# Optimization experiments

Hardware: AMD Instinct MI355X
Metric: run time of the kernel (lower is better)

The kernel has to match this reference:

```python
import math
import jax, jax.numpy as jnp
import numpy as np

N_HEADS = 16
CHUNK = 64  # sqrt(S) block size for the Cron-Root (sqrt-decomposition) branch


def _chunked_causal_attention(q, k, v, chunk=CHUNK):
    """Exact causal softmax attention computed in sqrt-size query blocks.

    Math-equivalent to F.scaled_dot_product_attention(q,k,v,is_causal=True),
    but never materializes the full [B,H,S,S] score matrix (honors the
    sqrt-decomposition structure of cron_root_attention_v14).
    q,k,v: [B,H,S,D] -> out [B,H,S,D]
    """
    B, H, S, D = q.shape
    scale = 1.0 / math.sqrt(D)
    nc = S // chunk
    qc = jnp.moveaxis(q.reshape(B, H, nc, chunk, D), 2, 0)  # [nc,B,H,C,D]
    kpos = jnp.arange(S)

    def body(_, inp):
        qi, ci = inp  # qi: [B,H,C,D], ci: scalar chunk index
        scores = jnp.einsum('bhcd,bhsd->bhcs', qi, k) * scale  # [B,H,C,S]
        qpos = ci * chunk + jnp.arange(chunk)
        mask = kpos[None, :] <= qpos[:, None]  # [C,S] causal
        scores = jnp.where(mask, scores, jnp.finfo(scores.dtype).min)
        p = jax.nn.softmax(scores, axis=-1)
        return None, jnp.einsum('bhcs,bhsd->bhcd', p, v)

    _, outs = jax.lax.scan(body, None, (qc, jnp.arange(nc)))  # [nc,B,H,C,D]
    return jnp.moveaxis(outs, 0, 2).reshape(B, H, S, D)


def setup_inputs() -> dict:
    key = jax.random.key(0)
    kx, kq, kk, kv, ko = jax.random.split(key, 5)
    d = 1024
    x = jax.random.normal(kx, (1, 4096, d), dtype=jnp.float32)
    # nn.Linear weights are [out_features, in_features]; no bias (bias=False)
    Wq = jax.random.normal(kq, (d, d), dtype=jnp.float32) * 0.02
    Wk = jax.random.normal(kk, (d, d), dtype=jnp.float32) * 0.02
    Wv = jax.random.normal(kv, (d, d), dtype=jnp.float32) * 0.02
    Wo = jax.random.normal(ko, (d, d), dtype=jnp.float32) * 0.02
    return {"x": x, "Wq": Wq, "Wk": Wk, "Wv": Wv, "Wo": Wo}


def reference(x, Wq, Wk, Wv, Wo):
    B, S, D = x.shape
    H = N_HEADS
    hd = D // H
    # projections (torch Linear: y = x @ W.T)
    q = (x @ Wq.T).reshape(B, S, H, hd).transpose(0, 2, 1, 3)
    k = (x @ Wk.T).reshape(B, S, H, hd).transpose(0, 2, 1, 3)
    v = (x @ Wv.T).reshape(B, S, H, hd).transpose(0, 2, 1, 3)
    # S=4096 >= threshold=1536 -> cron_root branch (exact causal attention)
    out = _chunked_causal_attention(q, k, v)
    out = out.transpose(0, 2, 1, 3).reshape(B, S, D)
    return out @ Wo.T
```

## Files before the change

### kernel.cpp

```cpp
#include <hip/hip_runtime.h>
#include <math.h>

#define S_LEN  4096
#define DMODEL 1024
#define NH     16
#define HD     64

typedef __bf16 bf16;
typedef __attribute__((ext_vector_type(8))) __bf16 bf16x8;
typedef __attribute__((ext_vector_type(4))) float  f32x4;

__device__ inline void gl_lds16(const void* g, void* l) {
    __builtin_amdgcn_global_load_lds(
        (const __attribute__((address_space(1))) void*)g,
        (__attribute__((address_space(3))) void*)l, 16, 0, 0);
}

__global__ __launch_bounds__(256)
void f32_to_bf16_all(const float* __restrict__ x,  const float* __restrict__ wq,
                     const float* __restrict__ wk, const float* __restrict__ wv,
                     const float* __restrict__ wo,
                     bf16* __restrict__ xb,  bf16* __restrict__ wqb,
                     bf16* __restrict__ wkb, bf16* __restrict__ wvb,
                     bf16* __restrict__ wob)
{
    int b = blockIdx.x;
    const float* s; bf16* d; int idx;
    if      (b < 2048) { s = x;  d = xb;  idx = b; }
    else if (b < 2560) { s = wq; d = wqb; idx = b - 2048; }
    else if (b < 3072) { s = wk; d = wkb; idx = b - 2560; }
    else if (b < 3584) { s = wv; d = wvb; idx = b - 3072; }
    else               { s = wo; d = wob; idx = b - 3584; }
    size_t e0 = ((size_t)idx * 256 + threadIdx.x) * 8;
    float4 a = *(const float4*)(s + e0);
    float4 c = *(const float4*)(s + e0 + 4);
    bf16x8 r;
    r[0] = (bf16)a.x; r[1] = (bf16)a.y; r[2] = (bf16)a.z; r[3] = (bf16)a.w;
    r[4] = (bf16)c.x; r[5] = (bf16)c.y; r[6] = (bf16)c.z; r[7] = (bf16)c.w;
    *(bf16x8*)(d + e0) = r;
}

template <typename OutT>
__device__ inline void gemm_body(const bf16* __restrict__ A, const bf16* __restrict__ B,
                                 OutT* __restrict__ C, bool trans, int M, int N, int K)
{
    __shared__ __align__(16) bf16 As[2][128 * 32];
    __shared__ __align__(16) bf16 Bs[2][128 * 32];

    const int t = threadIdx.x, lane = t & 63, w = t >> 6;
    const int m0 = blockIdx.x * 128, n0 = blockIdx.y * 128;
    const int wr = (w >> 1) * 64, wc = (w & 1) * 64;
    const int fr = lane & 15, fc = lane >> 4;

    const int  srow = w * 32 + (lane >> 2);
    const int  schk = (lane & 3) * 8;
    const bf16* Ag = A + (size_t)(m0 + srow) * K + schk;
    const bf16* Bg = B + (size_t)(n0 + srow) * K + schk;
    const int  sbase = (w * 32) * 32;

    f32x4 acc[4][4] = {};

    auto stage = [&](int buf, int k0) {
        gl_lds16(Ag + k0,                  &As[buf][sbase]);
        gl_lds16(Ag + k0 + (size_t)16 * K, &As[buf][sbase + 16 * 32]);
        gl_lds16(Bg + k0,                  &Bs[buf][sbase]);
        gl_lds16(Bg + k0 + (size_t)16 * K, &Bs[buf][sbase + 16 * 32]);
    };

    stage(0, 0);
    __syncthreads();
    int cur = 0;
    for (int k0 = 0; k0 < K; k0 += 32) {
        if (k0 + 32 < K) stage(cur ^ 1, k0 + 32);
        bf16x8 af[4], bv[4];
        #pragma unroll
        for (int fm = 0; fm < 4; ++fm)
            af[fm] = *(const bf16x8*)&As[cur][(wr + fm * 16 + fr) * 32 + fc * 8];
        #pragma unroll
        for (int fn = 0; fn < 4; ++fn)
            bv[fn] = *(const bf16x8*)&Bs[cur][(wc + fn * 16 + fr) * 32 + fc * 8];
        #pragma unroll
        for (int fm = 0; fm < 4; ++fm)
            #pragma unroll
            for (int fn = 0; fn < 4; ++fn)
                acc[fm][fn] = __builtin_amdgcn_mfma_f32_16x16x32_bf16(
                                  af[fm], bv[fn], acc[fm][fn], 0, 0, 0);
        __syncthreads();
        cur ^= 1;
    }

    #pragma unroll
    for (int fm = 0; fm < 4; ++fm)
        #pragma unroll
        for (int fn = 0; fn < 4; ++fn)
            #pragma unroll
            for (int r = 0; r < 4; ++r) {
                int row = m0 + wr + fm * 16 + fc * 4 + r;
                int col = n0 + wc + fn * 16 + fr;
                float v = acc[fm][fn][r];
                if (trans) C[(size_t)col * M + row] = (OutT)v;
                else       C[(size_t)row * N + col] = (OutT)v;
            }
}

__global__ __launch_bounds__(256)
void gemm_qkv(const bf16* __restrict__ A,
              const bf16* __restrict__ Wq, const bf16* __restrict__ Wk,
              const bf16* __restrict__ Wv,
              bf16* __restrict__ Qo, bf16* __restrict__ Ko, bf16* __restrict__ Vo)
{
    const int z = blockIdx.z;
    const bf16* B = (z == 0) ? Wq : (z == 1) ? Wk : Wv;
    bf16*       C = (z == 0) ? Qo : (z == 1) ? Ko : Vo;
    gemm_body<bf16>(A, B, C, z == 2, S_LEN, DMODEL, DMODEL);
}

__global__ __launch_bounds__(256)
void gemm_out(const bf16* __restrict__ A, const bf16* __restrict__ B,
              float* __restrict__ C)
{
    gemm_body<float>(A, B, C, false, S_LEN, DMODEL, DMODEL);
}

__global__ __launch_bounds__(256)
void attn_mfma(const bf16* __restrict__ Q, const bf16* __restrict__ Kb,
               const bf16* __restrict__ Vt, bf16* __restrict__ O)
{
    __shared__ __align__(16) bf16 Ks[2][64 * 64];
    __shared__ __align__(16) bf16 Vs[2][64 * 64];
    __shared__ __align__(16) bf16 Ps[4][16 * 64];

    const int t = threadIdx.x, lane = t & 63, w = t >> 6;
    const int h  = blockIdx.x & (NH - 1);
    const int j  = (int)(blockIdx.x >> 4);
    const int a  = j & 15, sg = j >> 4;
    const int qi = (sg == 0) ? a : (sg == 1) ? 63 - a : (sg == 2) ? 16 + a : 47 - a;
    const int qbase = qi * 64;
    const int fr = lane & 15, fc = lane >> 4;

    bf16x8 qf[2];
    #pragma unroll
    for (int kh = 0; kh < 2; ++kh)
        qf[kh] = *(const bf16x8*)(Q + (size_t)(qbase + w * 16 + fr) * DMODEL
                                    + h * HD + kh * 32 + fc * 8);

    f32x4 o[4] = {};
    float lsum[4] = {0.f, 0.f, 0.f, 0.f};

    auto stage = [&](int buf, int kb2) {
        const int kbase2 = kb2 * 64;
        #pragma unroll
        for (int i = 0; i < 2; ++i) {
            int row = w * 16 + i * 8 + (lane >> 3);
            int gch = (lane & 7) ^ (row & 7);
            gl_lds16(Kb + (size_t)(kbase2 + row) * DMODEL + h * HD + gch * 8,
                     &Ks[buf][(w * 16 + i * 8) * 64]);
            gl_lds16(Vt + (size_t)(h * HD + row) * S_LEN + kbase2 + gch * 8,
                     &Vs[buf][(w * 16 + i * 8) * 64]);
        }
    };

    stage(0, 0);
    __syncthreads();

    int cur = 0;
    for (int kb = 0; kb <= qi; ++kb) {
        if (kb < qi) stage(cur ^ 1, kb + 1);

        f32x4 s[4] = {};
        #pragma unroll
        for (int fn = 0; fn < 4; ++fn)
            #pragma unroll
            for (int kh = 0; kh < 2; ++kh) {
                bf16x8 kf = *(const bf16x8*)
                    &Ks[cur][(fn * 16 + fr) * 64 + (((kh * 4 + fc) ^ (fr & 7)) * 8)];
                s[fn] = __builtin_amdgcn_mfma_f32_16x16x32_bf16(qf[kh], kf, s[fn], 0, 0, 0);
            }

        if (kb == qi) {
            #pragma unroll
            for (int fn = 0; fn < 4; ++fn)
                #pragma unroll
                for (int r = 0; r < 4; ++r)
                    if (fn * 16 + fr > w * 16 + fc * 4 + r) s[fn][r] = -INFINITY;
        }

        #pragma unroll
        for (int fn = 0; fn < 4; ++fn)
            #pragma unroll
            for (int r = 0; r < 4; ++r) {
                float p = exp2f(s[fn][r] * 0.18033688011112042f);
                lsum[r] += p;
                int row  = fc * 4 + r;
                int slot = (fn * 2 + (fr >> 3)) ^ (row & 7);
                Ps[w][row * 64 + slot * 8 + (fr & 7)] = (bf16)p;
            }

        #pragma unroll
        for (int kvh = 0; kvh < 2; ++kvh) {
            bf16x8 pa = *(const bf16x8*)
                &Ps[w][fr * 64 + (((kvh * 4 + fc) ^ (fr & 7)) * 8)];
            #pragma unroll
            for (int fd = 0; fd < 4; ++fd) {
                bf16x8 vf = *(const bf16x8*)
                    &Vs[cur][(fd * 16 + fr) * 64 + (((kvh * 4 + fc) ^ (fr & 7)) * 8)];
                o[fd] = __builtin_amdgcn_mfma_f32_16x16x32_bf16(pa, vf, o[fd], 0, 0, 0);
            }
        }

        __syncthreads();
        cur ^= 1;
    }

    #pragma unroll
    for (int m = 1; m < 16; m <<= 1)
        #pragma unroll
        for (int r = 0; r < 4; ++r)
            lsum[r] += __shfl_xor(lsum[r], m, 64);

    #pragma unroll
    for (int fd = 0; fd < 4; ++fd)
        #pragma unroll
        for (int r = 0; r < 4; ++r) {
            int row = qbase + w * 16 + fc * 4 + r;
            int col = h * HD + fd * 16 + fr;
            O[(size_t)row * DMODEL + col] = (bf16)(o[fd][r] / lsum[r]);
        }
}

extern "C" void kernel_launch(void* const* d_in, const int* in_sizes, int n_in,
                              void* d_out, int out_size, void* d_ws, size_t ws_size,
                              hipStream_t stream)
{
    const float* x  = (const float*)d_in[0];
    const float* Wq = (const float*)d_in[1];
    const float* Wk = (const float*)d_in[2];
    const float* Wv = (const float*)d_in[3];
    const float* Wo = (const float*)d_in[4];

    const size_t M1 = 1024 * 1024;
    bf16* xb  = (bf16*)d_ws;
    bf16* wqb = xb  + 4 * M1;
    bf16* wkb = wqb + M1;
    bf16* wvb = wkb + M1;
    bf16* wob = wvb + M1;
    bf16* Qb  = wob + M1;
    bf16* Kb  = Qb  + 4 * M1;
    bf16* Vt  = Kb  + 4 * M1;
    bf16* Ob  = Vt  + 4 * M1;

    f32_to_bf16_all<<<4096, 256, 0, stream>>>(x, Wq, Wk, Wv, Wo,
                                              xb, wqb, wkb, wvb, wob);

    gemm_qkv<<<dim3(S_LEN / 128, DMODEL / 128, 3), 256, 0, stream>>>(
        xb, wqb, wkb, wvb, Qb, Kb, Vt);

    attn_mfma<<<dim3((S_LEN / 64) * NH), 256, 0, stream>>>(Qb, Kb, Vt, Ob);

    gemm_out<<<dim3(S_LEN / 128, DMODEL / 128), 256, 0, stream>>>(
        Ob, wob, (float*)d_out);
}
```

Measured before the change: 228.9 us.

## Keep attention probabilities in registers via transposed MFMA, drop LDS P staging

```diff
diff --git a/kernel.cpp b/kernel.cpp
--- a/kernel.cpp
+++ b/kernel.cpp
@@ -8,6 +8,7 @@
 
 typedef __bf16 bf16;
 typedef __attribute__((ext_vector_type(8))) __bf16 bf16x8;
+typedef __attribute__((ext_vector_type(4))) __bf16 bf16x4;
 typedef __attribute__((ext_vector_type(4))) float  f32x4;
 
 __device__ inline void gl_lds16(const void* g, void* l) {
@@ -128,7 +129,6 @@
 {
     __shared__ __align__(16) bf16 Ks[2][64 * 64];
     __shared__ __align__(16) bf16 Vs[2][64 * 64];
-    __shared__ __align__(16) bf16 Ps[4][16 * 64];
 
     const int t = threadIdx.x, lane = t & 63, w = t >> 6;
     const int h  = blockIdx.x & (NH - 1);
@@ -145,7 +145,7 @@
                                     + h * HD + kh * 32 + fc * 8);
 
     f32x4 o[4] = {};
-    float lsum[4] = {0.f, 0.f, 0.f, 0.f};
+    float lsum = 0.f;
 
     auto stage = [&](int buf, int kb2) {
         const int kbase2 = kb2 * 64;
@@ -174,7 +174,7 @@
             for (int kh = 0; kh < 2; ++kh) {
                 bf16x8 kf = *(const bf16x8*)
                     &Ks[cur][(fn * 16 + fr) * 64 + (((kh * 4 + fc) ^ (fr & 7)) * 8)];
-                s[fn] = __builtin_amdgcn_mfma_f32_16x16x32_bf16(qf[kh], kf, s[fn], 0, 0, 0);
+                s[fn] = __builtin_amdgcn_mfma_f32_16x16x32_bf16(kf, qf[kh], s[fn], 0, 0, 0);
             }
 
         if (kb == qi) {
@@ -182,7 +182,7 @@
             for (int fn = 0; fn < 4; ++fn)
                 #pragma unroll
                 for (int r = 0; r < 4; ++r)
-                    if (fn * 16 + fr > w * 16 + fc * 4 + r) s[fn][r] = -INFINITY;
+                    if (fn * 16 + fc * 4 + r > w * 16 + fr) s[fn][r] = -INFINITY;
         }
 
         #pragma unroll
@@ -190,21 +190,29 @@
             #pragma unroll
             for (int r = 0; r < 4; ++r) {
                 float p = exp2f(s[fn][r] * 0.18033688011112042f);
-                lsum[r] += p;
-                int row  = fc * 4 + r;
-                int slot = (fn * 2 + (fr >> 3)) ^ (row & 7);
-                Ps[w][row * 64 + slot * 8 + (fr & 7)] = (bf16)p;
+                lsum += p;
+                s[fn][r] = p;
             }
 
         #pragma unroll
         for (int kvh = 0; kvh < 2; ++kvh) {
-            bf16x8 pa = *(const bf16x8*)
-                &Ps[w][fr * 64 + (((kvh * 4 + fc) ^ (fr & 7)) * 8)];
+            bf16x8 pa;
+            #pragma unroll
+            for (int r = 0; r < 4; ++r) {
+                pa[r]     = (bf16)s[2 * kvh][r];
+                pa[4 + r] = (bf16)s[2 * kvh + 1][r];
+            }
             #pragma unroll
             for (int fd = 0; fd < 4; ++fd) {
-                bf16x8 vf = *(const bf16x8*)
-                    &Vs[cur][(fd * 16 + fr) * 64 + (((kvh * 4 + fc) ^ (fr & 7)) * 8)];
-                o[fd] = __builtin_amdgcn_mfma_f32_16x16x32_bf16(pa, vf, o[fd], 0, 0, 0);
+                const int rowb = (fd * 16 + fr) * 64 + (fc & 1) * 4;
+                bf16x4 va = *(const bf16x4*)
+                    &Vs[cur][rowb + (((kvh * 4     + (fc >> 1)) ^ (fr & 7)) * 8)];
+                bf16x4 vb = *(const bf16x4*)
+                    &Vs[cur][rowb + (((kvh * 4 + 2 + (fc >> 1)) ^ (fr & 7)) * 8)];
+                bf16x8 vf;
+                #pragma unroll
+                for (int e = 0; e < 4; ++e) { vf[e] = va[e]; vf[4 + e] = vb[e]; }
+                o[fd] = __builtin_amdgcn_mfma_f32_16x16x32_bf16(vf, pa, o[fd], 0, 0, 0);
             }
         }
 
@@ -212,20 +220,18 @@
         cur ^= 1;
     }
 
+    lsum += __shfl_xor(lsum, 16, 64);
+    lsum += __shfl_xor(lsum, 32, 64);
+    const float inv = 1.0f / lsum;
+
     #pragma unroll
-    for (int m = 1; m < 16; m <<= 1)
-        #pragma unroll
-        for (int r = 0; r < 4; ++r)
-            lsum[r] += __shfl_xor(lsum[r], m, 64);
-
-    #pragma unroll
-    for (int fd = 0; fd < 4; ++fd)
-        #pragma unroll
-        for (int r = 0; r < 4; ++r) {
-            int row = qbase + w * 16 + fc * 4 + r;
-            int col = h * HD + fd * 16 + fr;
-            O[(size_t)row * DMODEL + col] = (bf16)(o[fd][r] / lsum[r]);
-        }
+    for (int fd = 0; fd < 4; ++fd) {
+        bf16x4 ov;
+        #pragma unroll
+        for (int r = 0; r < 4; ++r) ov[r] = (bf16)(o[fd][r] * inv);
+        *(bf16x4*)(O + (size_t)(qbase + w * 16 + fr) * DMODEL
+                     + h * HD + fd * 16 + fc * 4) = ov;
+    }
 }
 
 extern "C" void kernel_launch(void* const* d_in, const int* in_sizes, int n_in,
```

Result: no change. 225.0 us (-1.7%).
